# Kernel tuning notes

Measured on AMD Instinct MI355X. Metric: run time of the kernel, lower is better.

The kernel has to match this reference:

```python
import jax, jax.numpy as jnp
import numpy as np


def setup_inputs() -> dict:
    key = jax.random.key(0)
    k1, k2 = jax.random.split(key)
    pred = jax.random.normal(k1, (1, 2048, 512), dtype=jnp.float32)
    cand = jax.random.normal(k2, (1, 65536, 512), dtype=jnp.float32)
    return {
        "predicted_transaction_company": pred,
        "future_transaction_companies_inc_current_data": cand,
    }


def reference(predicted_transaction_company, future_transaction_companies_inc_current_data):
    # torch.cdist with p=2 on [1,P,D] x [1,R,D] -> [1,P,R]; squeeze(0) -> [P,R]; global min.
    x = predicted_transaction_company[0]                       # [P, D]
    y = future_transaction_companies_inc_current_data[0]       # [R, D]
    sq = (
        jnp.sum(x * x, axis=-1)[:, None]
        + jnp.sum(y * y, axis=-1)[None, :]
        - 2.0 * jnp.einsum("pd,rd->pr", x, y)
    )                                                          # [P, R]
    distances = jnp.sqrt(jnp.maximum(sq, 0.0))
    return jnp.min(distances)
```

## Files before the change

### kernel.cpp

```cpp
#include <hip/hip_runtime.h>
#include <stdint.h>

#define P 2048
#define R 65536
#define DD 512
#define BT 128
#define BK 64

typedef __attribute__((ext_vector_type(8))) short short8;
typedef __attribute__((ext_vector_type(4))) float f32x4;

__device__ inline unsigned short f2bf(float f) {
  unsigned int u = __float_as_uint(f);
  u += 0x7fffu + ((u >> 16) & 1u);
  return (unsigned short)(u >> 16);
}

__device__ inline void gload_lds16(const void* g, void* l) {
  __builtin_amdgcn_global_load_lds(
      (const __attribute__((address_space(1))) unsigned int*)g,
      (__attribute__((address_space(3))) unsigned int*)l,
      16, 0, 0);
}

__global__ __launch_bounds__(256) void k_convert(
    const float* __restrict__ pred, const float* __restrict__ cand,
    unsigned short* __restrict__ Abf, unsigned short* __restrict__ Bbf,
    float* __restrict__ nx, float* __restrict__ ny,
    unsigned int* __restrict__ minp)
{
  if (blockIdx.x == 0 && threadIdx.x == 0) *minp = 0x7f800000u;
  int gw   = (blockIdx.x * 256 + threadIdx.x) >> 6;
  int lane = threadIdx.x & 63;
  if (gw >= P + R) return;
  const float* src; unsigned short* dst; float* np;
  if (gw < P) { src = pred + (size_t)gw * DD; dst = Abf + (size_t)gw * DD; np = nx + gw; }
  else { int r = gw - P; src = cand + (size_t)r * DD; dst = Bbf + (size_t)r * DD; np = ny + r; }
  const float4* s4 = ((const float4*)src) + lane * 2;
  float4 v0 = s4[0], v1 = s4[1];
  float ss = v0.x*v0.x + v0.y*v0.y + v0.z*v0.z + v0.w*v0.w
           + v1.x*v1.x + v1.y*v1.y + v1.z*v1.z + v1.w*v1.w;
  union { unsigned short h[8]; uint4 v; } pk;
  pk.h[0]=f2bf(v0.x); pk.h[1]=f2bf(v0.y); pk.h[2]=f2bf(v0.z); pk.h[3]=f2bf(v0.w);
  pk.h[4]=f2bf(v1.x); pk.h[5]=f2bf(v1.y); pk.h[6]=f2bf(v1.z); pk.h[7]=f2bf(v1.w);
  *(uint4*)(dst + (size_t)lane * 8) = pk.v;
  #pragma unroll
  for (int off = 32; off; off >>= 1) ss += __shfl_down(ss, off, 64);
  if (lane == 0) *np = ss;
}

__global__ __launch_bounds__(256) void k_gemm_min(
    const unsigned short* __restrict__ Abf, const unsigned short* __restrict__ Bbf,
    const float* __restrict__ nx, const float* __restrict__ ny,
    unsigned int* __restrict__ minp)
{
  __shared__ __align__(16) unsigned short As[BT * BK];
  __shared__ __align__(16) unsigned short Bs[BT * BK];
  __shared__ float wmin[4];

  const int tid  = threadIdx.x;
  const int wave = tid >> 6;
  const int lane = tid & 63;
  const int by = blockIdx.x & 15;
  const int bx = blockIdx.x >> 4;
  const int rowA0 = by * BT, rowB0 = bx * BT;
  const int wr = wave >> 1, wc = wave & 1;

  f32x4 zero = {0.f, 0.f, 0.f, 0.f};
  f32x4 acc[4][4];
  #pragma unroll
  for (int i = 0; i < 4; ++i)
    #pragma unroll
    for (int j = 0; j < 4; ++j) acc[i][j] = zero;

  const int rloc = lane >> 3;
  const int cswz = (lane & 7) ^ rloc;
  const unsigned short* gA[4]; const unsigned short* gB[4];
  unsigned short* lA[4]; unsigned short* lB[4];
  #pragma unroll
  for (int t = 0; t < 4; ++t) {
    const int rr = (wave * 4 + t) * 8 + rloc;
    gA[t] = Abf + (size_t)(rowA0 + rr) * DD + cswz * 8;
    gB[t] = Bbf + (size_t)(rowB0 + rr) * DD + cswz * 8;
    lA[t] = As + (wave * 4 + t) * 512;
    lB[t] = Bs + (wave * 4 + t) * 512;
  }

  const int m = lane & 15, quad = lane >> 4, mb = m & 7;
  const unsigned short* apB = As + (wr * 64 + m) * BK;
  const unsigned short* bpB = Bs + (wc * 64 + m) * BK;
  const int sw0 = ((quad    ) ^ mb) * 8;
  const int sw1 = ((quad + 4) ^ mb) * 8;

  for (int k0 = 0; k0 < DD; k0 += BK) {
    #pragma unroll
    for (int t = 0; t < 4; ++t) {
      gload_lds16(gA[t] + k0, lA[t]);
      gload_lds16(gB[t] + k0, lB[t]);
    }
    __syncthreads();

    short8 af[4], bfr[4];
    #pragma unroll
    for (int i = 0; i < 4; ++i) af[i]  = *(const short8*)(apB + i * 16 * BK + sw0);
    #pragma unroll
    for (int j = 0; j < 4; ++j) bfr[j] = *(const short8*)(bpB + j * 16 * BK + sw0);
    #pragma unroll
    for (int i = 0; i < 4; ++i)
      #pragma unroll
      for (int j = 0; j < 4; ++j)
        acc[i][j] = __builtin_amdgcn_mfma_f32_16x16x32_bf16(af[i], bfr[j], acc[i][j], 0, 0, 0);
    #pragma unroll
    for (int i = 0; i < 4; ++i) af[i]  = *(const short8*)(apB + i * 16 * BK + sw1);
    #pragma unroll
    for (int j = 0; j < 4; ++j) bfr[j] = *(const short8*)(bpB + j * 16 * BK + sw1);
    #pragma unroll
    for (int i = 0; i < 4; ++i)
      #pragma unroll
      for (int j = 0; j < 4; ++j)
        acc[i][j] = __builtin_amdgcn_mfma_f32_16x16x32_bf16(af[i], bfr[j], acc[i][j], 0, 0, 0);
    __syncthreads();
  }

  const int n16 = lane & 15;
  float lmin = 3.4e38f;
  #pragma unroll
  for (int i = 0; i < 4; ++i) {
    const int mbase = rowA0 + wr * 64 + i * 16 + quad * 4;
    float4 nxv = *(const float4*)(nx + mbase);
    #pragma unroll
    for (int j = 0; j < 4; ++j) {
      const int n = rowB0 + wc * 64 + j * 16 + n16;
      const float nyv = ny[n];
      f32x4 a = acc[i][j];
      lmin = fminf(lmin, nxv.x + nyv - 2.0f * a[0]);
      lmin = fminf(lmin, nxv.y + nyv - 2.0f * a[1]);
      lmin = fminf(lmin, nxv.z + nyv - 2.0f * a[2]);
      lmin = fminf(lmin, nxv.w + nyv - 2.0f * a[3]);
    }
  }
  #pragma unroll
  for (int off = 32; off; off >>= 1) lmin = fminf(lmin, __shfl_down(lmin, off, 64));
  if (lane == 0) wmin[wave] = lmin;
  __syncthreads();
  if (tid == 0) {
    float mn = fminf(fminf(wmin[0], wmin[1]), fminf(wmin[2], wmin[3]));
    atomicMin(minp, __float_as_uint(fmaxf(mn, 0.0f)));
  }
}

__global__ __launch_bounds__(64) void k_initmin(unsigned int* minp) {
  if (threadIdx.x == 0) *minp = 0x7f800000u;
}

__global__ __launch_bounds__(256) void k_brute(
    const float* __restrict__ pred, const float* __restrict__ cand,
    unsigned int* __restrict__ minp)
{
  __shared__ float yrow[DD];
  __shared__ float wm[4];
  const int c = blockIdx.x;
  for (int i = threadIdx.x; i < DD; i += 256) yrow[i] = cand[(size_t)c * DD + i];
  __syncthreads();
  float lmin = 3.4e38f;
  for (int p = threadIdx.x; p < P; p += 256) {
    const float* xp = pred + (size_t)p * DD;
    float s = 0.f;
    for (int k = 0; k < DD; ++k) { float d = xp[k] - yrow[k]; s = fmaf(d, d, s); }
    lmin = fminf(lmin, s);
  }
  #pragma unroll
  for (int off = 32; off; off >>= 1) lmin = fminf(lmin, __shfl_down(lmin, off, 64));
  if ((threadIdx.x & 63) == 0) wm[threadIdx.x >> 6] = lmin;
  __syncthreads();
  if (threadIdx.x == 0) {
    float mn = fminf(fminf(wm[0], wm[1]), fminf(wm[2], wm[3]));
    atomicMin(minp, __float_as_uint(fmaxf(mn, 0.0f)));
  }
}

__global__ __launch_bounds__(64) void k_finalize(const unsigned int* minp, float* out) {
  if (threadIdx.x == 0) out[0] = sqrtf(__uint_as_float(*minp));
}

extern "C" void kernel_launch(void* const* d_in, const int* in_sizes, int n_in,
                              void* d_out, int out_size, void* d_ws, size_t ws_size,
                              hipStream_t stream) {
  const float* pred = (const float*)d_in[0];
  const float* cand = (const float*)d_in[1];
  float* out = (float*)d_out;

  unsigned int* minp = (unsigned int*)d_ws;
  float* wsf = (float*)d_ws;
  float* nx = wsf + 16;
  float* ny = nx + P;
  unsigned short* Abf = (unsigned short*)(ny + R);
  unsigned short* Bbf = Abf + (size_t)P * DD;
  const size_t need = (size_t)(16 + P + R) * 4 + ((size_t)P * DD + (size_t)R * DD) * 2;

  if (ws_size >= need) {
    const int rows = P + R;
    k_convert<<<rows / 4, 256, 0, stream>>>(pred, cand, Abf, Bbf, nx, ny, minp);
    k_gemm_min<<<(P / BT) * (R / BT), 256, 0, stream>>>(Abf, Bbf, nx, ny, minp);
  } else {
    k_initmin<<<1, 64, 0, stream>>>(minp);
    k_brute<<<R, 256, 0, stream>>>(pred, cand, minp);
  }
  k_finalize<<<1, 64, 0, stream>>>(minp, out);
}
```

Before: 398.5 us.

## Double-buffer LDS tiles in GEMM-min kernel and regroup block order

The GEMM-min kernel gets two LDS buffers per operand. The next K-slice is issued with global_load_lds into the spare buffer while MFMAs run on the current one, and there is now one barrier per iteration instead of two. Block IDs are also remapped so that groups of 8 candidate tiles sweep all 16 prediction tiles together, aiming for better L2 reuse. The cost is twice the LDS per block, which may lower occupancy, and correctness relies on the barrier waiting for the outstanding async LDS loads.

```diff
diff --git a/kernel.cpp b/kernel.cpp
--- a/kernel.cpp
+++ b/kernel.cpp
@@ -6,6 +6,7 @@
 #define DD 512
 #define BT 128
 #define BK 64
+#define HALF (BT * BK)
 
 typedef __attribute__((ext_vector_type(8))) short short8;
 typedef __attribute__((ext_vector_type(4))) float f32x4;
@@ -54,15 +55,17 @@
     const float* __restrict__ nx, const float* __restrict__ ny,
     unsigned int* __restrict__ minp)
 {
-  __shared__ __align__(16) unsigned short As[BT * BK];
-  __shared__ __align__(16) unsigned short Bs[BT * BK];
+  __shared__ __align__(16) unsigned short As[2 * HALF];
+  __shared__ __align__(16) unsigned short Bs[2 * HALF];
   __shared__ float wmin[4];
 
   const int tid  = threadIdx.x;
   const int wave = tid >> 6;
   const int lane = tid & 63;
-  const int by = blockIdx.x & 15;
-  const int bx = blockIdx.x >> 4;
+
+  const int id = blockIdx.x;
+  const int by = (id >> 3) & 15;
+  const int bx = ((id >> 7) << 3) | (id & 7);
   const int rowA0 = by * BT, rowB0 = bx * BT;
   const int wr = wave >> 1, wc = wave & 1;
 
@@ -92,34 +95,44 @@
   const int sw0 = ((quad    ) ^ mb) * 8;
   const int sw1 = ((quad + 4) ^ mb) * 8;
 
-  for (int k0 = 0; k0 < DD; k0 += BK) {
-    #pragma unroll
-    for (int t = 0; t < 4; ++t) {
-      gload_lds16(gA[t] + k0, lA[t]);
-      gload_lds16(gB[t] + k0, lB[t]);
+  #pragma unroll
+  for (int t = 0; t < 4; ++t) {
+    gload_lds16(gA[t], lA[t]);
+    gload_lds16(gB[t], lB[t]);
+  }
+
+  for (int it = 0; it < DD / BK; ++it) {
+    __syncthreads();
+    const int cur = (it & 1) * HALF;
+    if (it < DD / BK - 1) {
+      const int nxt = ((it + 1) & 1) * HALF;
+      const int k0 = (it + 1) * BK;
+      #pragma unroll
+      for (int t = 0; t < 4; ++t) {
+        gload_lds16(gA[t] + k0, lA[t] + nxt);
+        gload_lds16(gB[t] + k0, lB[t] + nxt);
+      }
     }
-    __syncthreads();
 
     short8 af[4], bfr[4];
     #pragma unroll
-    for (int i = 0; i < 4; ++i) af[i]  = *(const short8*)(apB + i * 16 * BK + sw0);
-    #pragma unroll
-    for (int j = 0; j < 4; ++j) bfr[j] = *(const short8*)(bpB + j * 16 * BK + sw0);
+    for (int i = 0; i < 4; ++i) af[i]  = *(const short8*)(apB + cur + i * 16 * BK + sw0);
+    #pragma unroll
+    for (int j = 0; j < 4; ++j) bfr[j] = *(const short8*)(bpB + cur + j * 16 * BK + sw0);
     #pragma unroll
     for (int i = 0; i < 4; ++i)
       #pragma unroll
       for (int j = 0; j < 4; ++j)
         acc[i][j] = __builtin_amdgcn_mfma_f32_16x16x32_bf16(af[i], bfr[j], acc[i][j], 0, 0, 0);
     #pragma unroll
-    for (int i = 0; i < 4; ++i) af[i]  = *(const short8*)(apB + i * 16 * BK + sw1);
-    #pragma unroll
-    for (int j = 0; j < 4; ++j) bfr[j] = *(const short8*)(bpB + j * 16 * BK + sw1);
+    for (int i = 0; i < 4; ++i) af[i]  = *(const short8*)(apB + cur + i * 16 * BK + sw1);
+    #pragma unroll
+    for (int j = 0; j < 4; ++j) bfr[j] = *(const short8*)(bpB + cur + j * 16 * BK + sw1);
     #pragma unroll
     for (int i = 0; i < 4; ++i)
       #pragma unroll
       for (int j = 0; j < 4; ++j)
         acc[i][j] = __builtin_amdgcn_mfma_f32_16x16x32_bf16(af[i], bfr[j], acc[i][j], 0, 0, 0);
-    __syncthreads();
   }
 
   const int n16 = lane & 15;
```

After: 515.5 us. +29.4%, slower.
